# Kernel tuning notes

Hardware: AMD Instinct MI355X
Metric: run time of the kernel (lower is better)

The kernel has to match this reference:

```python
import jax, jax.numpy as jnp
import numpy as np

N_NODES = 50000
N_EDGES = 800000
N_GRAPHS = 512
IN_CH = 64
HID = 64
NEG_SLOPE = 0.2  # PyG GATConv default


def leaky_relu(x):
    return jnp.where(x >= 0, x, NEG_SLOPE * x)


def gat_conv(x, src, dst, W, a_src, a_dst, bias):
    # x: [N, in]; src/dst: [E] (self-loops already included)
    h = x @ W                                   # [N, hid]
    # per-edge attention logits (heads=1)
    alpha_s = h @ a_src                         # [N]
    alpha_d = h @ a_dst                         # [N]
    logits = leaky_relu(alpha_s[src] + alpha_d[dst])   # [E]
    # segment softmax over destination nodes
    seg_max = jax.ops.segment_max(logits, dst, num_segments=N_NODES)
    seg_max = jnp.where(jnp.isfinite(seg_max), seg_max, 0.0)
    ex = jnp.exp(logits - seg_max[dst])
    denom = jax.ops.segment_sum(ex, dst, num_segments=N_NODES)
    alpha = ex / jnp.maximum(denom[dst], 1e-16)
    # scatter-weighted aggregation of source features
    out = jax.ops.segment_sum(alpha[:, None] * h[src], dst, num_segments=N_NODES)
    return out + bias


def setup_inputs() -> dict:
    key = jax.random.key(0)
    ks = jax.random.split(key, 12)
    x = jax.random.normal(ks[0], (N_NODES, IN_CH), dtype=jnp.float32)
    edge_index = jax.random.randint(ks[1], (2, N_EDGES), 0, N_NODES, dtype=jnp.int64)
    batch = jnp.sort(jax.random.randint(ks[2], (N_NODES,), 0, N_GRAPHS, dtype=jnp.int64))
    s1 = 1.0 / np.sqrt(IN_CH)
    s2 = 1.0 / np.sqrt(HID)
    W1 = jax.random.normal(ks[3], (IN_CH, HID), dtype=jnp.float32) * s1
    a_src1 = jax.random.normal(ks[4], (HID,), dtype=jnp.float32) * s2
    a_dst1 = jax.random.normal(ks[5], (HID,), dtype=jnp.float32) * s2
    b1 = jnp.zeros((HID,), dtype=jnp.float32)
    W2 = jax.random.normal(ks[6], (HID, HID), dtype=jnp.float32) * s2
    a_src2 = jax.random.normal(ks[7], (HID,), dtype=jnp.float32) * s2
    a_dst2 = jax.random.normal(ks[8], (HID,), dtype=jnp.float32) * s2
    b2 = jnp.zeros((HID,), dtype=jnp.float32)
    return {"x": x, "edge_index": edge_index, "batch": batch,
            "W1": W1, "a_src1": a_src1, "a_dst1": a_dst1, "b1": b1,
            "W2": W2, "a_src2": a_src2, "a_dst2": a_dst2, "b2": b2}


def reference(x, edge_index, batch, W1, a_src1, a_dst1, b1, W2, a_src2, a_dst2, b2):
    # add self-loops (PyG GATConv default add_self_loops=True)
    loops = jnp.arange(N_NODES, dtype=edge_index.dtype)
    src = jnp.concatenate([edge_index[0], loops])
    dst = jnp.concatenate([edge_index[1], loops])
    h = jax.nn.elu(gat_conv(x, src, dst, W1, a_src1, a_dst1, b1))
    h = jax.nn.elu(gat_conv(h, src, dst, W2, a_src2, a_dst2, b2))
    # global mean pool per graph
    sums = jax.ops.segment_sum(h, batch, num_segments=N_GRAPHS)        # [G, hid]
    cnt = jax.ops.segment_sum(jnp.ones((N_NODES,), h.dtype), batch, num_segments=N_GRAPHS)
    return sums / jnp.maximum(cnt, 1.0)[:, None]
```

## Files before the change

### kernel.cpp

```cpp
#include <hip/hip_runtime.h>
#include <hip/hip_bf16.h>
#include <math.h>

#define N_NODES_C 50000
#define N_EDGES_C 800000
#define E_TOT_C   (N_EDGES_C + N_NODES_C)
#define N_GRAPHS_C 512
#define CH 64
#define NBUCK 391
#define NB_BUCK 256
#define BCAP 3328
#define TRF_NODES 64
#define NB_TRF ((N_NODES_C + TRF_NODES - 1) / TRF_NODES)

__device__ __forceinline__ float wave_reduce_sum(float v) {
#pragma unroll
    for (int m = 32; m >= 1; m >>= 1) v += __shfl_xor(v, m, 64);
    return v;
}

__device__ __forceinline__ void fma8(float wv, uint4 u, float* a) {
    a[0] = fmaf(wv, __uint_as_float(u.x << 16), a[0]);
    a[1] = fmaf(wv, __uint_as_float(u.x & 0xFFFF0000u), a[1]);
    a[2] = fmaf(wv, __uint_as_float(u.y << 16), a[2]);
    a[3] = fmaf(wv, __uint_as_float(u.y & 0xFFFF0000u), a[3]);
    a[4] = fmaf(wv, __uint_as_float(u.z << 16), a[4]);
    a[5] = fmaf(wv, __uint_as_float(u.z & 0xFFFF0000u), a[5]);
    a[6] = fmaf(wv, __uint_as_float(u.w << 16), a[6]);
    a[7] = fmaf(wv, __uint_as_float(u.w & 0xFFFF0000u), a[7]);
}


struct __align__(16) TrfSmem {
    __align__(16) float Wl[64][68];
    __align__(16) float xs[64][68];
    float wsv[64], wdv[64];
};
struct BuildSmem { int cnt[NBUCK]; int lbase[NBUCK]; };
union __align__(16) FusedSmem { TrfSmem t; BuildSmem b; };


__device__ __forceinline__ void build_body(
    BuildSmem& sm, int blk, const int* __restrict__ ei,
    int* __restrict__ bucket_cnt, unsigned int* __restrict__ buck_edges)
{
    int t = threadIdx.x;
    for (int i = t; i < NBUCK; i += 256) sm.cnt[i] = 0;
    __syncthreads();
    const int CHUNK = (E_TOT_C + NB_BUCK - 1) / NB_BUCK;
    int beg = blk * CHUNK, end = min(beg + CHUNK, E_TOT_C);
    for (int e = beg + t; e < end; e += 256) {
        int d = (e < N_EDGES_C) ? ei[N_EDGES_C + e] : (e - N_EDGES_C);
        atomicAdd(&sm.cnt[d >> 7], 1);
    }
    __syncthreads();
    for (int b = t; b < NBUCK; b += 256) {
        int c = sm.cnt[b];
        sm.lbase[b] = (c > 0) ? atomicAdd(&bucket_cnt[b], c) : 0;
        sm.cnt[b] = 0;
    }
    __syncthreads();
    for (int e = beg + t; e < end; e += 256) {
        int s_, d_;
        if (e < N_EDGES_C) { s_ = ei[e]; d_ = ei[N_EDGES_C + e]; }
        else               { s_ = d_ = e - N_EDGES_C; }
        int b = d_ >> 7;
        int pos = sm.lbase[b] + atomicAdd(&sm.cnt[b], 1);
        buck_edges[b * BCAP + pos] = ((unsigned)(d_ & 127) << 16) | (unsigned)s_;
    }
}


__device__ __forceinline__ void transform_body(
    TrfSmem& sm, int bb,
    const float* __restrict__ xin, const float* __restrict__ W,
    const float* __restrict__ a_s, const float* __restrict__ a_d,
    __hip_bfloat16* __restrict__ hout, float* __restrict__ as_out,
    float* __restrict__ ad_out)
{
    int t = threadIdx.x;
    const float4* W4 = (const float4*)W;
    for (int i = t; i < 1024; i += 256) {
        int row = i >> 4, f4 = i & 15;
        *reinterpret_cast<float4*>(&sm.Wl[row][f4 * 4]) = W4[i];
    }
    int n0 = bb * TRF_NODES;
    int nn = min(TRF_NODES, N_NODES_C - n0);
    if (nn < TRF_NODES) {
        for (int idx = t; idx < 64 * TRF_NODES; idx += 256) {
            int k = idx >> 6, row = idx & 63;
            if (row >= nn) sm.xs[k][row] = 0.f;
        }
    }
    for (int idx = t; idx < nn * 16; idx += 256) {
        int row = idx >> 4, f4 = idx & 15;
        float4 v = *reinterpret_cast<const float4*>(xin + (size_t)(n0 + row) * CH + f4 * 4);
        sm.xs[f4 * 4 + 0][row] = v.x;
        sm.xs[f4 * 4 + 1][row] = v.y;
        sm.xs[f4 * 4 + 2][row] = v.z;
        sm.xs[f4 * 4 + 3][row] = v.w;
    }
    __syncthreads();
    if (t < 64) {
        float ss = 0.f, dd = 0.f;
#pragma unroll 8
        for (int c2 = 0; c2 < 64; ++c2) {
            float wv = sm.Wl[t][c2];
            ss = fmaf(wv, a_s[c2], ss);
            dd = fmaf(wv, a_d[c2], dd);
        }
        sm.wsv[t] = ss; sm.wdv[t] = dd;
    }
    int w = t >> 6, c = t & 63, lane = t & 63;
    int r0 = w * 16;
    float acc[16];
#pragma unroll
    for (int i = 0; i < 16; ++i) acc[i] = 0.f;
#pragma unroll 8
    for (int k = 0; k < 64; ++k) {
        float wl = sm.Wl[k][c];
        const float4* xp = reinterpret_cast<const float4*>(&sm.xs[k][r0]);
        float4 xa = xp[0], xb = xp[1], xc = xp[2], xd = xp[3];
        acc[0]  = fmaf(xa.x, wl, acc[0]);  acc[1]  = fmaf(xa.y, wl, acc[1]);
        acc[2]  = fmaf(xa.z, wl, acc[2]);  acc[3]  = fmaf(xa.w, wl, acc[3]);
        acc[4]  = fmaf(xb.x, wl, acc[4]);  acc[5]  = fmaf(xb.y, wl, acc[5]);
        acc[6]  = fmaf(xb.z, wl, acc[6]);  acc[7]  = fmaf(xb.w, wl, acc[7]);
        acc[8]  = fmaf(xc.x, wl, acc[8]);  acc[9]  = fmaf(xc.y, wl, acc[9]);
        acc[10] = fmaf(xc.z, wl, acc[10]); acc[11] = fmaf(xc.w, wl, acc[11]);
        acc[12] = fmaf(xd.x, wl, acc[12]); acc[13] = fmaf(xd.y, wl, acc[13]);
        acc[14] = fmaf(xd.z, wl, acc[14]); acc[15] = fmaf(xd.w, wl, acc[15]);
    }
    size_t hb = (size_t)(n0 + r0) * CH + c;
#pragma unroll
    for (int i = 0; i < 16; ++i)
        if (r0 + i < nn) hout[hb + (size_t)i * CH] = __float2bfloat16(acc[i]);
    __syncthreads();
    int kb = lane & 3;
    int rloc = r0 + (lane >> 2);
    float ps = 0.f, pd = 0.f;
#pragma unroll
    for (int j = 0; j < 16; ++j) {
        int k = kb + 4 * j;
        float xv = sm.xs[k][rloc];
        ps = fmaf(xv, sm.wsv[k], ps);
        pd = fmaf(xv, sm.wdv[k], pd);
    }
    ps += __shfl_xor(ps, 1, 64); ps += __shfl_xor(ps, 2, 64);
    pd += __shfl_xor(pd, 1, 64); pd += __shfl_xor(pd, 2, 64);
    if (kb == 0 && rloc < nn) {
        as_out[n0 + rloc] = ps;
        ad_out[n0 + rloc] = pd;
    }
}


__global__ __launch_bounds__(256) void fused_build_trf(
    const int* __restrict__ ei, int* __restrict__ bucket_cnt,
    unsigned int* __restrict__ buck_edges,
    const float* __restrict__ xin, const float* __restrict__ W,
    const float* __restrict__ a_s, const float* __restrict__ a_d,
    __hip_bfloat16* __restrict__ hout, float* __restrict__ as_out,
    float* __restrict__ ad_out)
{
    __shared__ FusedSmem sm;
    if (blockIdx.x < NB_BUCK)
        build_body(sm.b, blockIdx.x, ei, bucket_cnt, buck_edges);
    else
        transform_body(sm.t, blockIdx.x - NB_BUCK, xin, W, a_s, a_d, hout, as_out, ad_out);
}

__global__ __launch_bounds__(256) void transform_kernel(
    const float* __restrict__ xin, const float* __restrict__ W,
    const float* __restrict__ a_s, const float* __restrict__ a_d,
    __hip_bfloat16* __restrict__ hout, float* __restrict__ as_out,
    float* __restrict__ ad_out)
{
    __shared__ TrfSmem sm;
    transform_body(sm, blockIdx.x, xin, W, a_s, a_d, hout, as_out, ad_out);
}


__global__ __launch_bounds__(512) void bucket_to_csr(const unsigned int* __restrict__ buck_edges,
                                                     const int* __restrict__ bucket_cnt,
                                                     const int* __restrict__ batch,
                                                     unsigned short* __restrict__ csr_src,
                                                     unsigned int* __restrict__ row_ptr,
                                                     int* __restrict__ gstart) {
    __shared__ unsigned int ebuf[BCAP];
    __shared__ unsigned short sbuf[BCAP];
    __shared__ int deg[128], off[128], cur[128];
    __shared__ int wsum;
    int bb = blockIdx.x, t = threadIdx.x;
    if (bb < 196 && t < 256) {
        int i = bb * 256 + t;
        if (i < N_NODES_C) {
            int bcur = batch[i];
            int bprev = (i > 0) ? batch[i - 1] : -1;
            for (int g = bprev + 1; g <= bcur; ++g) gstart[g] = i;
            if (i == N_NODES_C - 1)
                for (int g = bcur + 1; g <= N_GRAPHS_C; ++g) gstart[g] = N_NODES_C;
        }
    }
    int base = bb * BCAP;
    int size = min(bucket_cnt[bb], BCAP);
    int node0 = bb << 7;
    int nnodes = min(128, N_NODES_C - node0);
    for (int i = t; i < size; i += 512) ebuf[i] = buck_edges[base + i];
    if (t < 128) deg[t] = 0;
    __syncthreads();
    for (int i = t; i < size; i += 512) atomicAdd(&deg[(ebuf[i] >> 16) & 127], 1);
    __syncthreads();
    int myscan = 0;
    if (t < 128) {
        int l = t & 63;
        int s = deg[t];
#pragma unroll
        for (int o = 1; o < 64; o <<= 1) {
            int u = __shfl_up(s, o, 64);
            if (l >= o) s += u;
        }
        myscan = s;
        if (t == 63) wsum = s;
    }
    __syncthreads();
    if (t < 128) {
        int add = (t >= 64) ? wsum : 0;
        off[t] = myscan + add - deg[t];
        cur[t] = 0;
    }
    __syncthreads();
    for (int i = t; i < size; i += 512) {
        unsigned pk = ebuf[i];
        int l = (pk >> 16) & 127;
        int p = atomicAdd(&cur[l], 1);
        sbuf[off[l] + p] = (unsigned short)(pk & 0xFFFFu);
    }
    __syncthreads();
    for (int i = t; i < size; i += 512) csr_src[base + i] = sbuf[i];
    if (t < nnodes)
        row_ptr[node0 + t] = ((unsigned)(base + off[t]) << 8) | (unsigned)min(deg[t], 255);
}


__global__ __launch_bounds__(256) void aggregate_kernel(
    const __hip_bfloat16* __restrict__ h, const float* __restrict__ as,
    const float* __restrict__ ad, const float* __restrict__ bias,
    const unsigned int* __restrict__ row_ptr, const unsigned short* __restrict__ csr_src,
    float* __restrict__ out)
{
    int t = threadIdx.x;
    int w = t >> 6, lane = t & 63;
    int n = blockIdx.x * 4 + w;
    unsigned rp = row_ptr[n];
    float adn = ad[n];
    int beg = (int)(rp >> 8);
    int deg = (int)(rp & 255u);
    int sub = lane >> 3;
    int cg  = (lane & 7) << 3;
    int ch  = cg | sub;
    if (deg <= 32) {
        float bch = bias[ch];
        int dm = deg - 1;
        int s_reg = (int)csr_src[beg + min(lane, dm)];
        float asv = as[s_reg];
        int e0 = sub, e1 = sub + 8;
        int s0 = __shfl(s_reg, min(e0, dm), 64);
        int s1 = __shfl(s_reg, min(e1, dm), 64);
        uint4 u0 = *reinterpret_cast<const uint4*>(h + (size_t)s0 * CH + cg);
        uint4 u1 = *reinterpret_cast<const uint4*>(h + (size_t)s1 * CH + cg);
        bool two = (deg > 16);
        int e2 = sub + 16, e3 = sub + 24;
        uint4 u2 = make_uint4(0, 0, 0, 0), u3 = make_uint4(0, 0, 0, 0);
        if (two) {
            int s2 = __shfl(s_reg, min(e2, dm), 64);
            int s3 = __shfl(s_reg, min(e3, dm), 64);
            u2 = *reinterpret_cast<const uint4*>(h + (size_t)s2 * CH + cg);
            u3 = *reinterpret_cast<const uint4*>(h + (size_t)s3 * CH + cg);
        }
        float v0 = asv + adn;
        v0 = (v0 >= 0.f) ? v0 : 0.2f * v0;
        float ex = (lane < deg) ? __expf(v0) : 0.f;
        float w0 = __shfl(ex, e0, 64), w1 = __shfl(ex, e1, 64);
        float ssum = wave_reduce_sum(ex);
        float a[8] = {0.f, 0.f, 0.f, 0.f, 0.f, 0.f, 0.f, 0.f};
        fma8(w0, u0, a); fma8(w1, u1, a);
        if (two) {
            float w2 = __shfl(ex, e2, 64), w3 = __shfl(ex, e3, 64);
            fma8(w2, u2, a); fma8(w3, u3, a);
        }
        float inv = 1.f / fmaxf(ssum, 1e-16f);
        bool hi5 = (lane & 32) != 0;
        float t0 = __shfl_xor(hi5 ? a[0] : a[4], 32, 64);
        float t1 = __shfl_xor(hi5 ? a[1] : a[5], 32, 64);
        float t2 = __shfl_xor(hi5 ? a[2] : a[6], 32, 64);
        float t3 = __shfl_xor(hi5 ? a[3] : a[7], 32, 64);
        float b0 = (hi5 ? a[4] : a[0]) + t0;
        float b1 = (hi5 ? a[5] : a[1]) + t1;
        float b2 = (hi5 ? a[6] : a[2]) + t2;
        float b3 = (hi5 ? a[7] : a[3]) + t3;
        bool hi4 = (lane & 16) != 0;
        float u0s = __shfl_xor(hi4 ? b0 : b2, 16, 64);
        float u1s = __shfl_xor(hi4 ? b1 : b3, 16, 64);
        float c0 = (hi4 ? b2 : b0) + u0s;
        float c1 = (hi4 ? b3 : b1) + u1s;
        bool hi3 = (lane & 8) != 0;
        float v1 = __shfl_xor(hi3 ? c0 : c1, 8, 64);
        float r  = (hi3 ? c1 : c0) + v1;
        float v = r * inv + bch;
        v = (v > 0.f) ? v : __expf(v) - 1.f;
        out[(size_t)n * CH + ch] = v;
    } else if (deg <= 64) {
        float bch = bias[ch];
        int s_reg = (int)csr_src[beg + min(lane, deg - 1)];
        float ex = 0.f;
        if (lane < deg) {
            float v = as[s_reg] + adn;
            v = (v >= 0.f) ? v : 0.2f * v;
            ex = __expf(v);
        }
        float ssum = wave_reduce_sum(ex);
        float inv = 1.f / fmaxf(ssum, 1e-16f);
        float a[8] = {0.f, 0.f, 0.f, 0.f, 0.f, 0.f, 0.f, 0.f};
        int full = deg >> 4, rem = deg & 15;
        for (int j = 0; j < full; ++j) {
            int e1 = j * 16 + sub;
            int e2 = e1 + 8;
            int   s1 = __shfl(s_reg, e1, 64);
            int   s2 = __shfl(s_reg, e2, 64);
            float w1 = __shfl(ex, e1, 64);
            float w2 = __shfl(ex, e2, 64);
            uint4 u1 = *reinterpret_cast<const uint4*>(h + (size_t)s1 * CH + cg);
            uint4 u2 = *reinterpret_cast<const uint4*>(h + (size_t)s2 * CH + cg);
            fma8(w1, u1, a); fma8(w2, u2, a);
        }
        if (rem) {
            int dm = deg - 1;
            int e1 = full * 16 + sub;
            int   s1 = __shfl(s_reg, min(e1, dm), 64);
            float w1 = __shfl(ex, e1, 64);
            uint4 u1 = *reinterpret_cast<const uint4*>(h + (size_t)s1 * CH + cg);
            fma8(w1, u1, a);
            if (rem > 8) {
                int e2 = e1 + 8;
                int   s2 = __shfl(s_reg, min(e2, dm), 64);
                float w2 = __shfl(ex, e2, 64);
                uint4 u2 = *reinterpret_cast<const uint4*>(h + (size_t)s2 * CH + cg);
                fma8(w2, u2, a);
            }
        }
        bool hi5 = (lane & 32) != 0;
        float t0 = __shfl_xor(hi5 ? a[0] : a[4], 32, 64);
        float t1 = __shfl_xor(hi5 ? a[1] : a[5], 32, 64);
        float t2 = __shfl_xor(hi5 ? a[2] : a[6], 32, 64);
        float t3 = __shfl_xor(hi5 ? a[3] : a[7], 32, 64);
        float b0 = (hi5 ? a[4] : a[0]) + t0;
        float b1 = (hi5 ? a[5] : a[1]) + t1;
        float b2 = (hi5 ? a[6] : a[2]) + t2;
        float b3 = (hi5 ? a[7] : a[3]) + t3;
        bool hi4 = (lane & 16) != 0;
        float u0s = __shfl_xor(hi4 ? b0 : b2, 16, 64);
        float u1s = __shfl_xor(hi4 ? b1 : b3, 16, 64);
        float c0 = (hi4 ? b2 : b0) + u0s;
        float c1 = (hi4 ? b3 : b1) + u1s;
        bool hi3 = (lane & 8) != 0;
        float v1 = __shfl_xor(hi3 ? c0 : c1, 8, 64);
        float r  = (hi3 ? c1 : c0) + v1;
        float v = r * inv + bch;
        v = (v > 0.f) ? v : __expf(v) - 1.f;
        out[(size_t)n * CH + ch] = v;
    } else {
        int end = beg + deg;
        float ssum = 0.f;
        for (int i = beg + lane; i < end; i += 64) {
            float v = as[csr_src[i]] + adn;
            v = (v >= 0.f) ? v : 0.2f * v;
            ssum += __expf(v);
        }
        ssum = wave_reduce_sum(ssum);
        float inv = 1.f / fmaxf(ssum, 1e-16f);
        float acc = 0.f;
        for (int i = beg; i < end; ++i) {
            int s = csr_src[i];
            float v = as[s] + adn;
            v = (v >= 0.f) ? v : 0.2f * v;
            float ww = __expf(v);
            acc = fmaf(ww, __bfloat162float(h[(size_t)s * CH + lane]), acc);
        }
        acc = acc * inv + bias[lane];
        out[(size_t)n * CH + lane] = (acc > 0.f) ? acc : __expf(acc) - 1.f;
    }
}


__global__ __launch_bounds__(256) void pool_kernel(
    const float* __restrict__ h, const int* __restrict__ gstart,
    float* __restrict__ out)
{
    __shared__ float red[4][64];
    int g = blockIdx.x;
    int t = threadIdx.x, w = t >> 6, lane = t & 63;
    int beg = gstart[g], end = gstart[g + 1];
    float acc = 0.f;
    for (int n = beg + w; n < end; n += 4) acc += h[n * CH + lane];
    red[w][lane] = acc;
    __syncthreads();
    if (w == 0) {
        float v = red[0][lane] + red[1][lane] + red[2][lane] + red[3][lane];
        float c = (float)(end - beg);
        out[g * CH + lane] = v / fmaxf(c, 1.f);
    }
}


extern "C" void kernel_launch(void* const* d_in, const int* in_sizes, int n_in,
                              void* d_out, int out_size, void* d_ws, size_t ws_size,
                              hipStream_t stream)
{
    const float* x   = (const float*)d_in[0];
    const int*   ei  = (const int*)d_in[1];
    const int*   bat = (const int*)d_in[2];
    const float* W1  = (const float*)d_in[3];
    const float* as1 = (const float*)d_in[4];
    const float* ad1 = (const float*)d_in[5];
    const float* b1  = (const float*)d_in[6];
    const float* W2  = (const float*)d_in[7];
    const float* as2 = (const float*)d_in[8];
    const float* ad2 = (const float*)d_in[9];
    const float* b2  = (const float*)d_in[10];
    float* out = (float*)d_out;

    char* ws = (char*)d_ws;
    size_t off = 0;
    auto alloc = [&](size_t bytes) -> void* {
        void* p = ws + off;
        off += (bytes + 255) & ~size_t(255);
        return p;
    };
    __hip_bfloat16* hbuf = (__hip_bfloat16*)alloc(sizeof(__hip_bfloat16) * N_NODES_C * CH);
    float* obuf    = (float*)alloc(sizeof(float) * N_NODES_C * CH);
    float* alpha_s = (float*)alloc(sizeof(float) * N_NODES_C);
    float* alpha_d = (float*)alloc(sizeof(float) * N_NODES_C);
    int*   bucket_cnt = (int*)alloc(sizeof(int) * NBUCK);
    unsigned int* buck_edges = (unsigned int*)alloc(sizeof(unsigned) * NBUCK * BCAP);
    unsigned short* csr_src  = (unsigned short*)alloc(sizeof(unsigned short) * NBUCK * BCAP);
    unsigned int* row_ptr    = (unsigned int*)alloc(sizeof(unsigned) * N_NODES_C);
    int*   gstart  = (int*)alloc(sizeof(int) * (N_GRAPHS_C + 1));

    const int NB_AGG = N_NODES_C / 4;

    hipMemsetAsync(bucket_cnt, 0, sizeof(int) * NBUCK, stream);
    fused_build_trf<<<NB_BUCK + NB_TRF, 256, 0, stream>>>(ei, bucket_cnt, buck_edges,
                                                          x, W1, as1, ad1,
                                                          hbuf, alpha_s, alpha_d);
    bucket_to_csr<<<NBUCK, 512, 0, stream>>>(buck_edges, bucket_cnt, bat,
                                             csr_src, row_ptr, gstart);

    aggregate_kernel<<<NB_AGG, 256, 0, stream>>>(hbuf, alpha_s, alpha_d, b1,
                                                 row_ptr, csr_src, obuf);
    transform_kernel<<<NB_TRF, 256, 0, stream>>>(obuf, W2, as2, ad2, hbuf, alpha_s, alpha_d);
    aggregate_kernel<<<NB_AGG, 256, 0, stream>>>(hbuf, alpha_s, alpha_d, b2,
                                                 row_ptr, csr_src, obuf);

    pool_kernel<<<N_GRAPHS_C, 256, 0, stream>>>(obuf, gstart, out);
}
```

Baseline: 175.0 us.

## Fuse layer-1 aggregation with layer-2 transform, and layer-2 aggregation with pooling

Layer-1 aggregation now writes its per-node outputs into shared memory, and the same block immediately applies the layer-2 linear transform and attention projections. This removes the fp32 intermediate round trip to global memory and one kernel launch. Layer-2 aggregation now adds each node's contribution into the graph mean with atomics, which removes the separate pool kernel and the write of the second obuf. The cost is per-node atomic contention on 512x64 outputs, an extra memset, and lower parallelism in the fused block: 32 nodes per 512-thread block, with each wave looping over 4 nodes.

```diff
diff --git a/kernel.cpp b/kernel.cpp
--- a/kernel.cpp
+++ b/kernel.cpp
@@ -12,6 +12,8 @@
 #define BCAP 3328
 #define TRF_NODES 64
 #define NB_TRF ((N_NODES_C + TRF_NODES - 1) / TRF_NODES)
+#define FAT_NODES 32
+#define NB_FAT ((N_NODES_C + FAT_NODES - 1) / FAT_NODES)
 
 __device__ __forceinline__ float wave_reduce_sum(float v) {
 #pragma unroll
@@ -28,6 +30,151 @@
     a[5] = fmaf(wv, __uint_as_float(u.z & 0xFFFF0000u), a[5]);
     a[6] = fmaf(wv, __uint_as_float(u.w << 16), a[6]);
     a[7] = fmaf(wv, __uint_as_float(u.w & 0xFFFF0000u), a[7]);
+}
+
+
+__device__ __forceinline__ float agg_node_value(
+    int n, int lane, const __hip_bfloat16* __restrict__ h,
+    const float* __restrict__ as, const float* __restrict__ ad,
+    const float* __restrict__ bias,
+    const unsigned int* __restrict__ row_ptr,
+    const unsigned short* __restrict__ csr_src, int& ch_out)
+{
+    unsigned rp = row_ptr[n];
+    float adn = ad[n];
+    int beg = (int)(rp >> 8);
+    int deg = (int)(rp & 255u);
+    int sub = lane >> 3;
+    int cg  = (lane & 7) << 3;
+    int ch  = cg | sub;
+    ch_out = ch;
+    if (deg <= 32) {
+        int dm = deg - 1;
+        int sA = (int)csr_src[beg + min(sub, dm)];
+        int sB = (int)csr_src[beg + min(sub + 8, dm)];
+        uint4 u0 = *reinterpret_cast<const uint4*>(h + (size_t)sA * CH + cg);
+        uint4 u1 = *reinterpret_cast<const uint4*>(h + (size_t)sB * CH + cg);
+        bool two = (deg > 16);
+        uint4 u2 = make_uint4(0, 0, 0, 0), u3 = make_uint4(0, 0, 0, 0);
+        if (two) {
+            int sC = (int)csr_src[beg + min(sub + 16, dm)];
+            int sD = (int)csr_src[beg + min(sub + 24, dm)];
+            u2 = *reinterpret_cast<const uint4*>(h + (size_t)sC * CH + cg);
+            u3 = *reinterpret_cast<const uint4*>(h + (size_t)sD * CH + cg);
+        }
+        int s_reg = (int)csr_src[beg + min(lane, dm)];
+        float v0 = as[s_reg] + adn;
+        v0 = (v0 >= 0.f) ? v0 : 0.2f * v0;
+        float ex = (lane < deg) ? __expf(v0) : 0.f;
+        float w0 = __shfl(ex, sub, 64);
+        float w1 = __shfl(ex, sub + 8, 64);
+        float ssum = wave_reduce_sum(ex);
+        float a[8] = {0.f, 0.f, 0.f, 0.f, 0.f, 0.f, 0.f, 0.f};
+        fma8(w0, u0, a); fma8(w1, u1, a);
+        if (two) {
+            float w2 = __shfl(ex, sub + 16, 64);
+            float w3 = __shfl(ex, sub + 24, 64);
+            fma8(w2, u2, a); fma8(w3, u3, a);
+        }
+        float inv = 1.f / fmaxf(ssum, 1e-16f);
+        bool hi5 = (lane & 32) != 0;
+        float t0 = __shfl_xor(hi5 ? a[0] : a[4], 32, 64);
+        float t1 = __shfl_xor(hi5 ? a[1] : a[5], 32, 64);
+        float t2 = __shfl_xor(hi5 ? a[2] : a[6], 32, 64);
+        float t3 = __shfl_xor(hi5 ? a[3] : a[7], 32, 64);
+        float b0 = (hi5 ? a[4] : a[0]) + t0;
+        float b1 = (hi5 ? a[5] : a[1]) + t1;
+        float b2 = (hi5 ? a[6] : a[2]) + t2;
+        float b3 = (hi5 ? a[7] : a[3]) + t3;
+        bool hi4 = (lane & 16) != 0;
+        float u0s = __shfl_xor(hi4 ? b0 : b2, 16, 64);
+        float u1s = __shfl_xor(hi4 ? b1 : b3, 16, 64);
+        float c0 = (hi4 ? b2 : b0) + u0s;
+        float c1 = (hi4 ? b3 : b1) + u1s;
+        bool hi3 = (lane & 8) != 0;
+        float v1 = __shfl_xor(hi3 ? c0 : c1, 8, 64);
+        float r  = (hi3 ? c1 : c0) + v1;
+        float v = r * inv + bias[ch];
+        return (v > 0.f) ? v : __expf(v) - 1.f;
+    } else if (deg <= 64) {
+        int s_reg = (int)csr_src[beg + min(lane, deg - 1)];
+        float ex = 0.f;
+        if (lane < deg) {
+            float v = as[s_reg] + adn;
+            v = (v >= 0.f) ? v : 0.2f * v;
+            ex = __expf(v);
+        }
+        float ssum = wave_reduce_sum(ex);
+        float inv = 1.f / fmaxf(ssum, 1e-16f);
+        float a[8] = {0.f, 0.f, 0.f, 0.f, 0.f, 0.f, 0.f, 0.f};
+        int full = deg >> 4, rem = deg & 15;
+        for (int j = 0; j < full; ++j) {
+            int e1 = j * 16 + sub;
+            int e2 = e1 + 8;
+            int   s1 = __shfl(s_reg, e1, 64);
+            int   s2 = __shfl(s_reg, e2, 64);
+            float w1 = __shfl(ex, e1, 64);
+            float w2 = __shfl(ex, e2, 64);
+            uint4 u1 = *reinterpret_cast<const uint4*>(h + (size_t)s1 * CH + cg);
+            uint4 u2 = *reinterpret_cast<const uint4*>(h + (size_t)s2 * CH + cg);
+            fma8(w1, u1, a); fma8(w2, u2, a);
+        }
+        if (rem) {
+            int dm = deg - 1;
+            int e1 = full * 16 + sub;
+            int   s1 = __shfl(s_reg, min(e1, dm), 64);
+            float w1 = __shfl(ex, e1, 64);
+            uint4 u1 = *reinterpret_cast<const uint4*>(h + (size_t)s1 * CH + cg);
+            fma8(w1, u1, a);
+            if (rem > 8) {
+                int e2 = e1 + 8;
+                int   s2 = __shfl(s_reg, min(e2, dm), 64);
+                float w2 = __shfl(ex, e2, 64);
+                uint4 u2 = *reinterpret_cast<const uint4*>(h + (size_t)s2 * CH + cg);
+                fma8(w2, u2, a);
+            }
+        }
+        bool hi5 = (lane & 32) != 0;
+        float t0 = __shfl_xor(hi5 ? a[0] : a[4], 32, 64);
+        float t1 = __shfl_xor(hi5 ? a[1] : a[5], 32, 64);
+        float t2 = __shfl_xor(hi5 ? a[2] : a[6], 32, 64);
+        float t3 = __shfl_xor(hi5 ? a[3] : a[7], 32, 64);
+        float b0 = (hi5 ? a[4] : a[0]) + t0;
+        float b1 = (hi5 ? a[5] : a[1]) + t1;
+        float b2 = (hi5 ? a[6] : a[2]) + t2;
+        float b3 = (hi5 ? a[7] : a[3]) + t3;
+        bool hi4 = (lane & 16) != 0;
+        float u0s = __shfl_xor(hi4 ? b0 : b2, 16, 64);
+        float u1s = __shfl_xor(hi4 ? b1 : b3, 16, 64);
+        float c0 = (hi4 ? b2 : b0) + u0s;
+        float c1 = (hi4 ? b3 : b1) + u1s;
+        bool hi3 = (lane & 8) != 0;
+        float v1 = __shfl_xor(hi3 ? c0 : c1, 8, 64);
+        float r  = (hi3 ? c1 : c0) + v1;
+        float v = r * inv + bias[ch];
+        return (v > 0.f) ? v : __expf(v) - 1.f;
+    } else {
+        ch_out = lane;
+        int end = beg + deg;
+        float ssum = 0.f;
+        for (int i = beg + lane; i < end; i += 64) {
+            float v = as[csr_src[i]] + adn;
+            v = (v >= 0.f) ? v : 0.2f * v;
+            ssum += __expf(v);
+        }
+        ssum = wave_reduce_sum(ssum);
+        float inv = 1.f / fmaxf(ssum, 1e-16f);
+        float acc = 0.f;
+        for (int i = beg; i < end; ++i) {
+            int s = csr_src[i];
+            float v = as[s] + adn;
+            v = (v >= 0.f) ? v : 0.2f * v;
+            float ww = __expf(v);
+            acc = fmaf(ww, __bfloat162float(h[(size_t)s * CH + lane]), acc);
+        }
+        acc = acc * inv + bias[lane];
+        return (acc > 0.f) ? acc : __expf(acc) - 1.f;
+    }
 }
 
 
@@ -167,16 +314,6 @@
         build_body(sm.b, blockIdx.x, ei, bucket_cnt, buck_edges);
     else
         transform_body(sm.t, blockIdx.x - NB_BUCK, xin, W, a_s, a_d, hout, as_out, ad_out);
-}
-
-__global__ __launch_bounds__(256) void transform_kernel(
-    const float* __restrict__ xin, const float* __restrict__ W,
-    const float* __restrict__ a_s, const float* __restrict__ a_d,
-    __hip_bfloat16* __restrict__ hout, float* __restrict__ as_out,
-    float* __restrict__ ad_out)
-{
-    __shared__ TrfSmem sm;
-    transform_body(sm, blockIdx.x, xin, W, a_s, a_d, hout, as_out, ad_out);
 }
 
 
@@ -242,173 +379,110 @@
 }
 
 
-__global__ __launch_bounds__(256) void aggregate_kernel(
-    const __hip_bfloat16* __restrict__ h, const float* __restrict__ as,
-    const float* __restrict__ ad, const float* __restrict__ bias,
+struct __align__(16) FatSmem {
+    __align__(16) float Wl[64][68];
+    __align__(16) float xs[64][36];
+    float wsv[64], wdv[64];
+};
+
+__global__ __launch_bounds__(512) void fused_agg_trf(
+    const __hip_bfloat16* __restrict__ h1, const float* __restrict__ as1n,
+    const float* __restrict__ ad1n, const float* __restrict__ b1,
     const unsigned int* __restrict__ row_ptr, const unsigned short* __restrict__ csr_src,
+    const float* __restrict__ W2, const float* __restrict__ a_s2,
+    const float* __restrict__ a_d2,
+    __hip_bfloat16* __restrict__ hout2, float* __restrict__ as_out2,
+    float* __restrict__ ad_out2)
+{
+    __shared__ FatSmem sm;
+    int t = threadIdx.x, bb = blockIdx.x;
+    int wv = t >> 6, lane = t & 63;
+    int n0 = bb * FAT_NODES;
+    int nn = min(FAT_NODES, N_NODES_C - n0);
+    const float4* W4 = (const float4*)W2;
+    for (int i = t; i < 1024; i += 512) {
+        int row = i >> 4, f4 = i & 15;
+        *reinterpret_cast<float4*>(&sm.Wl[row][f4 * 4]) = W4[i];
+    }
+    if (nn < FAT_NODES) {
+        for (int idx = t; idx < 64 * FAT_NODES; idx += 512) {
+            int k = idx >> 5, row = idx & 31;
+            if (row >= nn) sm.xs[k][row] = 0.f;
+        }
+    }
+    for (int q = 0; q < 4; ++q) {
+        int nl = wv * 4 + q;
+        if (nl < nn) {
+            int ch;
+            float v = agg_node_value(n0 + nl, lane, h1, as1n, ad1n, b1,
+                                     row_ptr, csr_src, ch);
+            sm.xs[ch][nl] = v;
+        }
+    }
+    __syncthreads();
+    if (t < 64) {
+        float ss = 0.f, dd = 0.f;
+#pragma unroll 8
+        for (int c2 = 0; c2 < 64; ++c2) {
+            float wv2 = sm.Wl[t][c2];
+            ss = fmaf(wv2, a_s2[c2], ss);
+            dd = fmaf(wv2, a_d2[c2], dd);
+        }
+        sm.wsv[t] = ss; sm.wdv[t] = dd;
+    }
+    int c = lane;
+    int r0 = wv * 4;
+    float acc[4] = {0.f, 0.f, 0.f, 0.f};
+#pragma unroll 8
+    for (int k = 0; k < 64; ++k) {
+        float wl = sm.Wl[k][c];
+        float4 xa = *reinterpret_cast<const float4*>(&sm.xs[k][r0]);
+        acc[0] = fmaf(xa.x, wl, acc[0]);
+        acc[1] = fmaf(xa.y, wl, acc[1]);
+        acc[2] = fmaf(xa.z, wl, acc[2]);
+        acc[3] = fmaf(xa.w, wl, acc[3]);
+    }
+    size_t hb = (size_t)(n0 + r0) * CH + c;
+#pragma unroll
+    for (int i = 0; i < 4; ++i)
+        if (r0 + i < nn) hout2[hb + (size_t)i * CH] = __float2bfloat16(acc[i]);
+    __syncthreads();
+    int kb = lane & 15;
+    int rloc = r0 + (lane >> 4);
+    float ps = 0.f, pd = 0.f;
+#pragma unroll
+    for (int j = 0; j < 4; ++j) {
+        int k = kb + 16 * j;
+        float xv = sm.xs[k][rloc];
+        ps = fmaf(xv, sm.wsv[k], ps);
+        pd = fmaf(xv, sm.wdv[k], pd);
+    }
+    ps += __shfl_xor(ps, 1, 64); ps += __shfl_xor(ps, 2, 64);
+    ps += __shfl_xor(ps, 4, 64); ps += __shfl_xor(ps, 8, 64);
+    pd += __shfl_xor(pd, 1, 64); pd += __shfl_xor(pd, 2, 64);
+    pd += __shfl_xor(pd, 4, 64); pd += __shfl_xor(pd, 8, 64);
+    if (kb == 0 && rloc < nn) {
+        as_out2[n0 + rloc] = ps;
+        ad_out2[n0 + rloc] = pd;
+    }
+}
+
+
+__global__ __launch_bounds__(256) void agg_pool(
+    const __hip_bfloat16* __restrict__ h2, const float* __restrict__ as2n,
+    const float* __restrict__ ad2n, const float* __restrict__ b2,
+    const unsigned int* __restrict__ row_ptr, const unsigned short* __restrict__ csr_src,
+    const int* __restrict__ batch, const int* __restrict__ gstart,
     float* __restrict__ out)
 {
     int t = threadIdx.x;
     int w = t >> 6, lane = t & 63;
     int n = blockIdx.x * 4 + w;
-    unsigned rp = row_ptr[n];
-    float adn = ad[n];
-    int beg = (int)(rp >> 8);
-    int deg = (int)(rp & 255u);
-    int sub = lane >> 3;
-    int cg  = (lane & 7) << 3;
-    int ch  = cg | sub;
-    if (deg <= 32) {
-        float bch = bias[ch];
-        int dm = deg - 1;
-        int s_reg = (int)csr_src[beg + min(lane, dm)];
-        float asv = as[s_reg];
-        int e0 = sub, e1 = sub + 8;
-        int s0 = __shfl(s_reg, min(e0, dm), 64);
-        int s1 = __shfl(s_reg, min(e1, dm), 64);
-        uint4 u0 = *reinterpret_cast<const uint4*>(h + (size_t)s0 * CH + cg);
-        uint4 u1 = *reinterpret_cast<const uint4*>(h + (size_t)s1 * CH + cg);
-        bool two = (deg > 16);
-        int e2 = sub + 16, e3 = sub + 24;
-        uint4 u2 = make_uint4(0, 0, 0, 0), u3 = make_uint4(0, 0, 0, 0);
-        if (two) {
-            int s2 = __shfl(s_reg, min(e2, dm), 64);
-            int s3 = __shfl(s_reg, min(e3, dm), 64);
-            u2 = *reinterpret_cast<const uint4*>(h + (size_t)s2 * CH + cg);
-            u3 = *reinterpret_cast<const uint4*>(h + (size_t)s3 * CH + cg);
-        }
-        float v0 = asv + adn;
-        v0 = (v0 >= 0.f) ? v0 : 0.2f * v0;
-        float ex = (lane < deg) ? __expf(v0) : 0.f;
-        float w0 = __shfl(ex, e0, 64), w1 = __shfl(ex, e1, 64);
-        float ssum = wave_reduce_sum(ex);
-        float a[8] = {0.f, 0.f, 0.f, 0.f, 0.f, 0.f, 0.f, 0.f};
-        fma8(w0, u0, a); fma8(w1, u1, a);
-        if (two) {
-            float w2 = __shfl(ex, e2, 64), w3 = __shfl(ex, e3, 64);
-            fma8(w2, u2, a); fma8(w3, u3, a);
-        }
-        float inv = 1.f / fmaxf(ssum, 1e-16f);
-        bool hi5 = (lane & 32) != 0;
-        float t0 = __shfl_xor(hi5 ? a[0] : a[4], 32, 64);
-        float t1 = __shfl_xor(hi5 ? a[1] : a[5], 32, 64);
-        float t2 = __shfl_xor(hi5 ? a[2] : a[6], 32, 64);
-        float t3 = __shfl_xor(hi5 ? a[3] : a[7], 32, 64);
-        float b0 = (hi5 ? a[4] : a[0]) + t0;
-        float b1 = (hi5 ? a[5] : a[1]) + t1;
-        float b2 = (hi5 ? a[6] : a[2]) + t2;
-        float b3 = (hi5 ? a[7] : a[3]) + t3;
-        bool hi4 = (lane & 16) != 0;
-        float u0s = __shfl_xor(hi4 ? b0 : b2, 16, 64);
-        float u1s = __shfl_xor(hi4 ? b1 : b3, 16, 64);
-        float c0 = (hi4 ? b2 : b0) + u0s;
-        float c1 = (hi4 ? b3 : b1) + u1s;
-        bool hi3 = (lane & 8) != 0;
-        float v1 = __shfl_xor(hi3 ? c0 : c1, 8, 64);
-        float r  = (hi3 ? c1 : c0) + v1;
-        float v = r * inv + bch;
-        v = (v > 0.f) ? v : __expf(v) - 1.f;
-        out[(size_t)n * CH + ch] = v;
-    } else if (deg <= 64) {
-        float bch = bias[ch];
-        int s_reg = (int)csr_src[beg + min(lane, deg - 1)];
-        float ex = 0.f;
-        if (lane < deg) {
-            float v = as[s_reg] + adn;
-            v = (v >= 0.f) ? v : 0.2f * v;
-            ex = __expf(v);
-        }
-        float ssum = wave_reduce_sum(ex);
-        float inv = 1.f / fmaxf(ssum, 1e-16f);
-        float a[8] = {0.f, 0.f, 0.f, 0.f, 0.f, 0.f, 0.f, 0.f};
-        int full = deg >> 4, rem = deg & 15;
-        for (int j = 0; j < full; ++j) {
-            int e1 = j * 16 + sub;
-            int e2 = e1 + 8;
-            int   s1 = __shfl(s_reg, e1, 64);
-            int   s2 = __shfl(s_reg, e2, 64);
-            float w1 = __shfl(ex, e1, 64);
-            float w2 = __shfl(ex, e2, 64);
-            uint4 u1 = *reinterpret_cast<const uint4*>(h + (size_t)s1 * CH + cg);
-            uint4 u2 = *reinterpret_cast<const uint4*>(h + (size_t)s2 * CH + cg);
-            fma8(w1, u1, a); fma8(w2, u2, a);
-        }
-        if (rem) {
-            int dm = deg - 1;
-            int e1 = full * 16 + sub;
-            int   s1 = __shfl(s_reg, min(e1, dm), 64);
-            float w1 = __shfl(ex, e1, 64);
-            uint4 u1 = *reinterpret_cast<const uint4*>(h + (size_t)s1 * CH + cg);
-            fma8(w1, u1, a);
-            if (rem > 8) {
-                int e2 = e1 + 8;
-                int   s2 = __shfl(s_reg, min(e2, dm), 64);
-                float w2 = __shfl(ex, e2, 64);
-                uint4 u2 = *reinterpret_cast<const uint4*>(h + (size_t)s2 * CH + cg);
-                fma8(w2, u2, a);
-            }
-        }
-        bool hi5 = (lane & 32) != 0;
-        float t0 = __shfl_xor(hi5 ? a[0] : a[4], 32, 64);
-        float t1 = __shfl_xor(hi5 ? a[1] : a[5], 32, 64);
-        float t2 = __shfl_xor(hi5 ? a[2] : a[6], 32, 64);
-        float t3 = __shfl_xor(hi5 ? a[3] : a[7], 32, 64);
-        float b0 = (hi5 ? a[4] : a[0]) + t0;
-        float b1 = (hi5 ? a[5] : a[1]) + t1;
-        float b2 = (hi5 ? a[6] : a[2]) + t2;
-        float b3 = (hi5 ? a[7] : a[3]) + t3;
-        bool hi4 = (lane & 16) != 0;
-        float u0s = __shfl_xor(hi4 ? b0 : b2, 16, 64);
-        float u1s = __shfl_xor(hi4 ? b1 : b3, 16, 64);
-        float c0 = (hi4 ? b2 : b0) + u0s;
-        float c1 = (hi4 ? b3 : b1) + u1s;
-        bool hi3 = (lane & 8) != 0;
-        float v1 = __shfl_xor(hi3 ? c0 : c1, 8, 64);
-        float r  = (hi3 ? c1 : c0) + v1;
-        float v = r * inv + bch;
-        v = (v > 0.f) ? v : __expf(v) - 1.f;
-        out[(size_t)n * CH + ch] = v;
-    } else {
-        int end = beg + deg;
-        float ssum = 0.f;
-        for (int i = beg + lane; i < end; i += 64) {
-            float v = as[csr_src[i]] + adn;
-            v = (v >= 0.f) ? v : 0.2f * v;
-            ssum += __expf(v);
-        }
-        ssum = wave_reduce_sum(ssum);
-        float inv = 1.f / fmaxf(ssum, 1e-16f);
-        float acc = 0.f;
-        for (int i = beg; i < end; ++i) {
-            int s = csr_src[i];
-            float v = as[s] + adn;
-            v = (v >= 0.f) ? v : 0.2f * v;
-            float ww = __expf(v);
-            acc = fmaf(ww, __bfloat162float(h[(size_t)s * CH + lane]), acc);
-        }
-        acc = acc * inv + bias[lane];
-        out[(size_t)n * CH + lane] = (acc > 0.f) ? acc : __expf(acc) - 1.f;
-    }
-}
-
-
-__global__ __launch_bounds__(256) void pool_kernel(
-    const float* __restrict__ h, const int* __restrict__ gstart,
-    float* __restrict__ out)
-{
-    __shared__ float red[4][64];
-    int g = blockIdx.x;
-    int t = threadIdx.x, w = t >> 6, lane = t & 63;
-    int beg = gstart[g], end = gstart[g + 1];
-    float acc = 0.f;
-    for (int n = beg + w; n < end; n += 4) acc += h[n * CH + lane];
-    red[w][lane] = acc;
-    __syncthreads();
-    if (w == 0) {
-        float v = red[0][lane] + red[1][lane] + red[2][lane] + red[3][lane];
-        float c = (float)(end - beg);
-        out[g * CH + lane] = v / fmaxf(c, 1.f);
-    }
+    int ch;
+    float v = agg_node_value(n, lane, h2, as2n, ad2n, b2, row_ptr, csr_src, ch);
+    int g = batch[n];
+    float cnt = (float)(gstart[g + 1] - gstart[g]);
+    atomicAdd(&out[g * CH + ch], v / fmaxf(cnt, 1.f));
 }
 
 
@@ -436,10 +510,12 @@
         off += (bytes + 255) & ~size_t(255);
         return p;
     };
-    __hip_bfloat16* hbuf = (__hip_bfloat16*)alloc(sizeof(__hip_bfloat16) * N_NODES_C * CH);
-    float* obuf    = (float*)alloc(sizeof(float) * N_NODES_C * CH);
-    float* alpha_s = (float*)alloc(sizeof(float) * N_NODES_C);
-    float* alpha_d = (float*)alloc(sizeof(float) * N_NODES_C);
+    __hip_bfloat16* hbuf1 = (__hip_bfloat16*)alloc(sizeof(__hip_bfloat16) * N_NODES_C * CH);
+    __hip_bfloat16* hbuf2 = (__hip_bfloat16*)alloc(sizeof(__hip_bfloat16) * N_NODES_C * CH);
+    float* as1n = (float*)alloc(sizeof(float) * N_NODES_C);
+    float* ad1n = (float*)alloc(sizeof(float) * N_NODES_C);
+    float* as2n = (float*)alloc(sizeof(float) * N_NODES_C);
+    float* ad2n = (float*)alloc(sizeof(float) * N_NODES_C);
     int*   bucket_cnt = (int*)alloc(sizeof(int) * NBUCK);
     unsigned int* buck_edges = (unsigned int*)alloc(sizeof(unsigned) * NBUCK * BCAP);
     unsigned short* csr_src  = (unsigned short*)alloc(sizeof(unsigned short) * NBUCK * BCAP);
@@ -449,17 +525,17 @@
     const int NB_AGG = N_NODES_C / 4;
 
     hipMemsetAsync(bucket_cnt, 0, sizeof(int) * NBUCK, stream);
+    hipMemsetAsync(out, 0, sizeof(float) * N_GRAPHS_C * CH, stream);
+
     fused_build_trf<<<NB_BUCK + NB_TRF, 256, 0, stream>>>(ei, bucket_cnt, buck_edges,
                                                           x, W1, as1, ad1,
-                                                          hbuf, alpha_s, alpha_d);
+                                                          hbuf1, as1n, ad1n);
     bucket_to_csr<<<NBUCK, 512, 0, stream>>>(buck_edges, bucket_cnt, bat,
                                              csr_src, row_ptr, gstart);
-
-    aggregate_kernel<<<NB_AGG, 256, 0, stream>>>(hbuf, alpha_s, alpha_d, b1,
-                                                 row_ptr, csr_src, obuf);
-    transform_kernel<<<NB_TRF, 256, 0, stream>>>(obuf, W2, as2, ad2, hbuf, alpha_s, alpha_d);
-    aggregate_kernel<<<NB_AGG, 256, 0, stream>>>(hbuf, alpha_s, alpha_d, b2,
-                                                 row_ptr, csr_src, obuf);
-
-    pool_kernel<<<N_GRAPHS_C, 256, 0, stream>>>(obuf, gstart, out);
-}
+    fused_agg_trf<<<NB_FAT, 512, 0, stream>>>(hbuf1, as1n, ad1n, b1,
+                                              row_ptr, csr_src,
+                                              W2, as2, ad2,
+                                              hbuf2, as2n, ad2n);
+    agg_pool<<<NB_AGG, 256, 0, stream>>>(hbuf2, as2n, ad2n, b2,
+                                         row_ptr, csr_src, bat, gstart, out);
+}
```

After: 180.7 us. 3.2% more time.
